# Optimization experiments

Hardware: AMD Instinct MI355X
Metric: run time of the kernel (lower is better)

## Reference

```python
import jax, jax.numpy as jnp
import numpy as np

N_NODES = 100000
N_GRAPHS = 512


def _gin_layer(x, src, dst, W, b):
    # GINConv with eps=0: nn((1+eps)*x + sum_{j in N(i)} x_j), then relu outside
    msgs = x[src]                                    # [E, D] gather
    agg = jax.ops.segment_sum(msgs, dst, num_segments=N_NODES)
    h = (x + agg) @ W + b
    return jax.nn.relu(h)


def setup_inputs() -> dict:
    key = jax.random.key(0)
    ks = jax.random.split(key, 12)
    in_c, hid, out_c = 128, 128, 64
    E = 1600000
    x = jax.random.normal(ks[0], (N_NODES, in_c), dtype=jnp.float32)
    edge_index = jax.random.randint(ks[1], (2, E), 0, N_NODES, dtype=jnp.int64)
    batch = jnp.sort(jax.random.randint(ks[2], (N_NODES,), 0, N_GRAPHS, dtype=jnp.int64))
    s = lambda d: 1.0 / jnp.sqrt(d)
    W1 = jax.random.uniform(ks[3], (in_c, hid), jnp.float32, -s(in_c), s(in_c))
    b1 = jax.random.uniform(ks[4], (hid,), jnp.float32, -s(in_c), s(in_c))
    W2 = jax.random.uniform(ks[5], (hid, hid), jnp.float32, -s(hid), s(hid))
    b2 = jax.random.uniform(ks[6], (hid,), jnp.float32, -s(hid), s(hid))
    W3 = jax.random.uniform(ks[7], (hid, hid), jnp.float32, -s(hid), s(hid))
    b3 = jax.random.uniform(ks[8], (hid,), jnp.float32, -s(hid), s(hid))
    Wfc = jax.random.uniform(ks[9], (hid, out_c), jnp.float32, -s(hid), s(hid))
    bfc = jax.random.uniform(ks[10], (out_c,), jnp.float32, -s(hid), s(hid))
    return {"x": x, "edge_index": edge_index, "batch": batch,
            "W1": W1, "b1": b1, "W2": W2, "b2": b2, "W3": W3, "b3": b3,
            "Wfc": Wfc, "bfc": bfc}


def reference(x, edge_index, batch, W1, b1, W2, b2, W3, b3, Wfc, bfc):
    src, dst = edge_index[0], edge_index[1]
    h = _gin_layer(x, src, dst, W1, b1)
    h = _gin_layer(h, src, dst, W2, b2)
    h = _gin_layer(h, src, dst, W3, b3)
    # global mean pool over graphs
    sums = jax.ops.segment_sum(h, batch, num_segments=N_GRAPHS)          # [G, D]
    counts = jax.ops.segment_sum(jnp.ones((h.shape[0],), h.dtype), batch,
                                 num_segments=N_GRAPHS)
    pooled = sums / jnp.maximum(counts, 1.0)[:, None]
    # dropout is identity at inference
    return pooled @ Wfc + bfc
```

## Files before the change

kernel.cpp:

```cpp
#include <hip/hip_runtime.h>

#define NNODES 100000
#define NGRAPHS 512
#define D 128
#define OUTC 64
#define NEDGES 1600000
#define SCAN_NB ((NNODES + 1 + 1023) / 1024)


__global__ void k_deg(const int* __restrict__ dst, int* __restrict__ deg, int E) {
    int e = blockIdx.x * 256 + threadIdx.x;
    if (e < E) atomicAdd(&deg[dst[e]], 1);
}

__global__ __launch_bounds__(1024) void k_scan1(const int* __restrict__ deg,
                                                int* __restrict__ off,
                                                int* __restrict__ bsum) {
    __shared__ int sm[1024];
    int t = threadIdx.x;
    int i = blockIdx.x * 1024 + t;
    int v = (i < NNODES) ? deg[i] : 0;
    sm[t] = v;
    __syncthreads();
    #pragma unroll
    for (int ofs = 1; ofs < 1024; ofs <<= 1) {
        int add = (t >= ofs) ? sm[t - ofs] : 0;
        __syncthreads();
        sm[t] += add;
        __syncthreads();
    }
    if (i <= NNODES) off[i] = sm[t] - v;
    if (t == 1023) bsum[blockIdx.x] = sm[1023];
}

__global__ __launch_bounds__(128) void k_scan2(int* __restrict__ bsum) {
    __shared__ int sm[128];
    int t = threadIdx.x;
    int v = (t < SCAN_NB) ? bsum[t] : 0;
    sm[t] = v;
    __syncthreads();
    #pragma unroll
    for (int ofs = 1; ofs < 128; ofs <<= 1) {
        int add = (t >= ofs) ? sm[t - ofs] : 0;
        __syncthreads();
        sm[t] += add;
        __syncthreads();
    }
    if (t < SCAN_NB) bsum[t] = sm[t] - v;
}

__global__ __launch_bounds__(1024) void k_scan3(int* __restrict__ off,
                                                const int* __restrict__ bsum) {
    int i = blockIdx.x * 1024 + threadIdx.x;
    if (i <= NNODES) off[i] += bsum[blockIdx.x];
}

__global__ void k_fill(const int* __restrict__ src, const int* __restrict__ dst,
                       const int* __restrict__ off, int* __restrict__ cur,
                       int* __restrict__ csr, int E) {
    int e = blockIdx.x * 256 + threadIdx.x;
    if (e < E) {
        int d = dst[e];
        int p = off[d] + atomicAdd(&cur[d], 1);
        csr[p] = src[e];
    }
}


__global__ __launch_bounds__(256, 6) void k_agg(
    const float* __restrict__ x, const int* __restrict__ off,
    const int* __restrict__ csr, float* __restrict__ agg) {
    int gid = blockIdx.x * 256 + threadIdx.x;
    int n = gid >> 5;
    if (n >= NNODES) return;
    int c = (gid & 31) << 2;

    float4 acc = *(const float4*)(x + (size_t)n * D + c);
    int o0 = off[n], o1 = off[n + 1];

    for (int j = o0; j < o1; j += 8) {
        int idx[8];
        float m[8];
        #pragma unroll
        for (int k = 0; k < 8; ++k) {
            int jj = j + k;
            bool ok = jj < o1;
            idx[k] = ok ? csr[jj] : n;
            m[k] = ok ? 1.f : 0.f;
        }
        float4 v[8];
        #pragma unroll
        for (int k = 0; k < 8; ++k)
            v[k] = *(const float4*)(x + (size_t)idx[k] * D + c);
        #pragma unroll
        for (int k = 0; k < 8; ++k) {
            acc.x = fmaf(v[k].x, m[k], acc.x);
            acc.y = fmaf(v[k].y, m[k], acc.y);
            acc.z = fmaf(v[k].z, m[k], acc.z);
            acc.w = fmaf(v[k].w, m[k], acc.w);
        }
    }
    *(float4*)(agg + (size_t)n * D + c) = acc;
}


__global__ __launch_bounds__(256, 4) void k_gemm(
    const float* __restrict__ xin, const float* __restrict__ W,
    const float* __restrict__ bias, float* __restrict__ hout) {
    __shared__ float xs[64 * 132];
    __shared__ float Wl[32 * 128];

    int t = threadIdx.x;
    int n0 = blockIdx.x * 64;

    for (int i = t; i < 64 * 32; i += 256) {
        int r = i >> 5, c4 = i & 31;
        int n = n0 + r;
        if (n > NNODES - 1) n = NNODES - 1;
        *(float4*)(xs + r * 132 + c4 * 4) =
            *(const float4*)(xin + (size_t)n * D + c4 * 4);
    }

    int cg = t & 31;
    int ng = t >> 5;
    float4 bv = *(const float4*)(bias + cg * 4);
    float acc[8][4];
    #pragma unroll
    for (int i = 0; i < 8; ++i) {
        acc[i][0] = bv.x; acc[i][1] = bv.y; acc[i][2] = bv.z; acc[i][3] = bv.w;
    }

    for (int q = 0; q < 4; ++q) {
        __syncthreads();
        for (int i = t; i < 32 * 32; i += 256) {
            int r = i >> 5, c4 = i & 31;
            *(float4*)(Wl + r * 128 + c4 * 4) =
                *(const float4*)(W + (size_t)(q * 32 + r) * D + c4 * 4);
        }
        __syncthreads();
        #pragma unroll
        for (int k4 = 0; k4 < 8; ++k4) {
            float4 w0 = *(const float4*)(Wl + (k4 * 4 + 0) * 128 + cg * 4);
            float4 w1 = *(const float4*)(Wl + (k4 * 4 + 1) * 128 + cg * 4);
            float4 w2 = *(const float4*)(Wl + (k4 * 4 + 2) * 128 + cg * 4);
            float4 w3 = *(const float4*)(Wl + (k4 * 4 + 3) * 128 + cg * 4);
            #pragma unroll
            for (int i = 0; i < 8; ++i) {
                float4 xv = *(const float4*)(xs + (ng * 8 + i) * 132 + q * 32 + k4 * 4);
                acc[i][0] += xv.x * w0.x + xv.y * w1.x + xv.z * w2.x + xv.w * w3.x;
                acc[i][1] += xv.x * w0.y + xv.y * w1.y + xv.z * w2.y + xv.w * w3.y;
                acc[i][2] += xv.x * w0.z + xv.y * w1.z + xv.z * w2.z + xv.w * w3.z;
                acc[i][3] += xv.x * w0.w + xv.y * w1.w + xv.z * w2.w + xv.w * w3.w;
            }
        }
    }

    #pragma unroll
    for (int i = 0; i < 8; ++i) {
        int n = n0 + ng * 8 + i;
        if (n < NNODES) {
            float4 o;
            o.x = fmaxf(acc[i][0], 0.f);
            o.y = fmaxf(acc[i][1], 0.f);
            o.z = fmaxf(acc[i][2], 0.f);
            o.w = fmaxf(acc[i][3], 0.f);
            *(float4*)(hout + (size_t)n * D + cg * 4) = o;
        }
    }
}


__global__ void k_goff(const int* __restrict__ batch, int* __restrict__ goff, int N) {
    int i = blockIdx.x * 256 + threadIdx.x;
    if (i >= N) return;
    int b = batch[i];
    if (i == 0) {
        for (int g = 0; g <= b; ++g) goff[g] = 0;
    } else {
        int p = batch[i - 1];
        for (int g = p + 1; g <= b; ++g) goff[g] = i;
    }
    if (i == N - 1) {
        for (int g = b + 1; g <= NGRAPHS; ++g) goff[g] = N;
    }
}


__global__ __launch_bounds__(128) void k_pool(const float* __restrict__ h,
                                              const int* __restrict__ goff,
                                              float* __restrict__ pooled) {
    int g = blockIdx.x, c = threadIdx.x;
    int s = goff[g], e = goff[g + 1];
    float a = 0.f;
    int n = s;
    for (; n + 4 <= e; n += 4) {
        float v0 = h[(size_t)(n + 0) * D + c];
        float v1 = h[(size_t)(n + 1) * D + c];
        float v2 = h[(size_t)(n + 2) * D + c];
        float v3 = h[(size_t)(n + 3) * D + c];
        a += (v0 + v1) + (v2 + v3);
    }
    for (; n < e; ++n) a += h[(size_t)n * D + c];
    pooled[(size_t)g * D + c] = a / fmaxf((float)(e - s), 1.f);
}


__global__ __launch_bounds__(64) void k_fc(const float* __restrict__ pooled,
                                           const float* __restrict__ Wfc,
                                           const float* __restrict__ bfc,
                                           float* __restrict__ out) {
    __shared__ float row[128];
    int g = blockIdx.x, o = threadIdx.x;
    row[o] = pooled[(size_t)g * D + o];
    row[o + 64] = pooled[(size_t)g * D + o + 64];
    __syncthreads();
    float a = bfc[o];
    #pragma unroll 8
    for (int k = 0; k < 128; ++k) a += row[k] * Wfc[k * OUTC + o];
    out[(size_t)g * OUTC + o] = a;
}


extern "C" void kernel_launch(void* const* d_in, const int* in_sizes, int n_in,
                              void* d_out, int out_size, void* d_ws, size_t ws_size,
                              hipStream_t stream) {
    const float* x = (const float*)d_in[0];
    const int* ei = (const int*)d_in[1];
    const int* batch = (const int*)d_in[2];
    const float* W1 = (const float*)d_in[3];
    const float* b1 = (const float*)d_in[4];
    const float* W2 = (const float*)d_in[5];
    const float* b2 = (const float*)d_in[6];
    const float* W3 = (const float*)d_in[7];
    const float* b3 = (const float*)d_in[8];
    const float* Wfc = (const float*)d_in[9];
    const float* bfc = (const float*)d_in[10];
    float* out = (float*)d_out;

    const int* src = ei;
    const int* dst = ei + NEDGES;

    char* ws = (char*)d_ws;
    size_t P = 0;
    auto alloc = [&](size_t bytes) {
        size_t r = P;
        P += (bytes + 255) & ~(size_t)255;
        return r;
    };
    int* off = (int*)(ws + alloc((NNODES + 2) * 4));
    int* deg = (int*)(ws + alloc(NNODES * 4));
    int* cur = (int*)(ws + alloc(NNODES * 4));
    int* bsum = (int*)(ws + alloc(SCAN_NB * 4));
    int* csr = (int*)(ws + alloc((size_t)(NEDGES + 64) * 4));
    float* bufA = (float*)(ws + alloc((size_t)NNODES * D * 4));
    float* bufB = (float*)(ws + alloc((size_t)NNODES * D * 4));
    float* pooled = (float*)(ws + alloc((size_t)NGRAPHS * D * 4));
    int* goff = (int*)(ws + alloc((NGRAPHS + 1) * 4));

    hipMemsetAsync(deg, 0, NNODES * 4, stream);
    hipMemsetAsync(cur, 0, NNODES * 4, stream);

    k_deg<<<NEDGES / 256, 256, 0, stream>>>(dst, deg, NEDGES);
    k_scan1<<<SCAN_NB, 1024, 0, stream>>>(deg, off, bsum);
    k_scan2<<<1, 128, 0, stream>>>(bsum);
    k_scan3<<<SCAN_NB, 1024, 0, stream>>>(off, bsum);
    k_fill<<<NEDGES / 256, 256, 0, stream>>>(src, dst, off, cur, csr, NEDGES);
    k_goff<<<(NNODES + 255) / 256, 256, 0, stream>>>(batch, goff, NNODES);

    const int AGG_GRID = (NNODES * 32 + 255) / 256;
    const int GEMM_GRID = (NNODES + 63) / 64;

    k_agg<<<AGG_GRID, 256, 0, stream>>>(x, off, csr, bufB);
    k_gemm<<<GEMM_GRID, 256, 0, stream>>>(bufB, W1, b1, bufA);
    k_agg<<<AGG_GRID, 256, 0, stream>>>(bufA, off, csr, bufB);
    k_gemm<<<GEMM_GRID, 256, 0, stream>>>(bufB, W2, b2, bufA);
    k_agg<<<AGG_GRID, 256, 0, stream>>>(bufA, off, csr, bufB);
    k_gemm<<<GEMM_GRID, 256, 0, stream>>>(bufB, W3, b3, bufA);

    k_pool<<<NGRAPHS, 128, 0, stream>>>(bufA, goff, pooled);
    k_fc<<<NGRAPHS, 64, 0, stream>>>(pooled, Wfc, bfc, out);
}
```

Before: 898.5 us.

## Fuse neighbor aggregation into GEMM kernel per GIN layer

Merges the separate aggregation and GEMM kernels into one per-layer kernel. Each block gathers and sums neighbor features for its 64 nodes straight into shared memory and then runs the existing GEMM tile. This removes the global write and re-read of the aggregated [N,128] buffer and three kernel launches. In exchange, the gather now runs at the GEMM kernel's occupancy (launch bounds 256,4 with large shared memory) rather than the dedicated agg kernel's (256,6), which may leave less latency hiding for the random gathers.

```diff
diff --git a/kernel.cpp b/kernel.cpp
--- a/kernel.cpp
+++ b/kernel.cpp
@@ -67,58 +67,48 @@
 }
 
 
-__global__ __launch_bounds__(256, 6) void k_agg(
-    const float* __restrict__ x, const int* __restrict__ off,
-    const int* __restrict__ csr, float* __restrict__ agg) {
-    int gid = blockIdx.x * 256 + threadIdx.x;
-    int n = gid >> 5;
-    if (n >= NNODES) return;
-    int c = (gid & 31) << 2;
-
-    float4 acc = *(const float4*)(x + (size_t)n * D + c);
-    int o0 = off[n], o1 = off[n + 1];
-
-    for (int j = o0; j < o1; j += 8) {
-        int idx[8];
-        float m[8];
-        #pragma unroll
-        for (int k = 0; k < 8; ++k) {
-            int jj = j + k;
-            bool ok = jj < o1;
-            idx[k] = ok ? csr[jj] : n;
-            m[k] = ok ? 1.f : 0.f;
-        }
-        float4 v[8];
-        #pragma unroll
-        for (int k = 0; k < 8; ++k)
-            v[k] = *(const float4*)(x + (size_t)idx[k] * D + c);
-        #pragma unroll
-        for (int k = 0; k < 8; ++k) {
-            acc.x = fmaf(v[k].x, m[k], acc.x);
-            acc.y = fmaf(v[k].y, m[k], acc.y);
-            acc.z = fmaf(v[k].z, m[k], acc.z);
-            acc.w = fmaf(v[k].w, m[k], acc.w);
-        }
-    }
-    *(float4*)(agg + (size_t)n * D + c) = acc;
-}
-
-
-__global__ __launch_bounds__(256, 4) void k_gemm(
-    const float* __restrict__ xin, const float* __restrict__ W,
+__global__ __launch_bounds__(256, 4) void k_layer(
+    const float* __restrict__ xin, const int* __restrict__ off,
+    const int* __restrict__ csr, const float* __restrict__ W,
     const float* __restrict__ bias, float* __restrict__ hout) {
     __shared__ float xs[64 * 132];
     __shared__ float Wl[32 * 128];
 
     int t = threadIdx.x;
     int n0 = blockIdx.x * 64;
-
-    for (int i = t; i < 64 * 32; i += 256) {
-        int r = i >> 5, c4 = i & 31;
-        int n = n0 + r;
+    int c = (t & 31) << 2;
+    int nl = t >> 5;
+
+    for (int p = 0; p < 8; ++p) {
+        int ln = p * 8 + nl;
+        int n = n0 + ln;
         if (n > NNODES - 1) n = NNODES - 1;
-        *(float4*)(xs + r * 132 + c4 * 4) =
-            *(const float4*)(xin + (size_t)n * D + c4 * 4);
+
+        float4 acc = *(const float4*)(xin + (size_t)n * D + c);
+        int o0 = off[n], o1 = off[n + 1];
+        for (int j = o0; j < o1; j += 8) {
+            int idx[8];
+            float m[8];
+            #pragma unroll
+            for (int k = 0; k < 8; ++k) {
+                int jj = j + k;
+                bool ok = jj < o1;
+                idx[k] = ok ? csr[jj] : n;
+                m[k] = ok ? 1.f : 0.f;
+            }
+            float4 v[8];
+            #pragma unroll
+            for (int k = 0; k < 8; ++k)
+                v[k] = *(const float4*)(xin + (size_t)idx[k] * D + c);
+            #pragma unroll
+            for (int k = 0; k < 8; ++k) {
+                acc.x = fmaf(v[k].x, m[k], acc.x);
+                acc.y = fmaf(v[k].y, m[k], acc.y);
+                acc.z = fmaf(v[k].z, m[k], acc.z);
+                acc.w = fmaf(v[k].w, m[k], acc.w);
+            }
+        }
+        *(float4*)(xs + ln * 132 + c) = acc;
     }
 
     int cg = t & 31;
@@ -267,15 +257,11 @@
     k_fill<<<NEDGES / 256, 256, 0, stream>>>(src, dst, off, cur, csr, NEDGES);
     k_goff<<<(NNODES + 255) / 256, 256, 0, stream>>>(batch, goff, NNODES);
 
-    const int AGG_GRID = (NNODES * 32 + 255) / 256;
-    const int GEMM_GRID = (NNODES + 63) / 64;
-
-    k_agg<<<AGG_GRID, 256, 0, stream>>>(x, off, csr, bufB);
-    k_gemm<<<GEMM_GRID, 256, 0, stream>>>(bufB, W1, b1, bufA);
-    k_agg<<<AGG_GRID, 256, 0, stream>>>(bufA, off, csr, bufB);
-    k_gemm<<<GEMM_GRID, 256, 0, stream>>>(bufB, W2, b2, bufA);
-    k_agg<<<AGG_GRID, 256, 0, stream>>>(bufA, off, csr, bufB);
-    k_gemm<<<GEMM_GRID, 256, 0, stream>>>(bufB, W3, b3, bufA);
+    const int LAYER_GRID = (NNODES + 63) / 64;
+
+    k_layer<<<LAYER_GRID, 256, 0, stream>>>(x, off, csr, W1, b1, bufA);
+    k_layer<<<LAYER_GRID, 256, 0, stream>>>(bufA, off, csr, W2, b2, bufB);
+    k_layer<<<LAYER_GRID, 256, 0, stream>>>(bufB, off, csr, W3, b3, bufA);
 
     k_pool<<<NGRAPHS, 128, 0, stream>>>(bufA, goff, pooled);
     k_fc<<<NGRAPHS, 64, 0, stream>>>(pooled, Wfc, bfc, out);
```

Result: faster. 825.1 us (-8.2%).
